# Optimization experiments

Measured on AMD Instinct MI355X. Metric: run time of the kernel, lower is better.

The kernel has to match this reference:

```python
import jax, jax.numpy as jnp
import numpy as np

H = 128          # hidden_dim
LATENT = 32
OUT = 2 * LATENT # diagonal output dist
S0, S1, S2, S3 = 65536, 16384, 4096, 1024  # HR grid, mesh0_hr/grid_lr, mesh1_hr/mesh0_lr, mesh2_hr/mesh1_lr
G = 15           # total stacked GNN blocks (HR: g2m, 2 up, 3x2 intra; LR cond: g2m, 1 up, 2x2 intra)
EDGES = {
    'hr_g2m': (131072, S0, S1), 'hr_m2m0': (131072, S1, S1),
    'hr_m2m1': (32768, S2, S2), 'hr_m2m2': (8192, S3, S3),
    'hr_up0': (65536, S1, S2), 'hr_up1': (16384, S2, S3),
    'lr_g2m': (65536, S1, S2), 'lr_m2m0': (32768, S2, S2),
    'lr_m2m1': (8192, S3, S3), 'lr_up0': (16384, S2, S3),
}


def setup_inputs():
    keys = iter(jax.random.split(jax.random.key(0), 80))
    inp = {}
    inp['high_emb'] = jax.random.normal(next(keys), (S0, H), jnp.float32)
    inp['low_emb'] = jax.random.normal(next(keys), (S1, H), jnp.float32)
    for name, n in [('hr_mesh0', S1), ('hr_mesh1', S2), ('hr_mesh2', S3), ('lr_mesh0', S2), ('lr_mesh1', S3)]:
        inp[name] = jax.random.normal(next(keys), (n, H), jnp.float32)
    for name, (e, ns, nr) in EDGES.items():
        inp[name + '_feat'] = jax.random.normal(next(keys), (e, H), jnp.float32)
        inp[name + '_src'] = jax.random.randint(next(keys), (e,), 0, ns, jnp.int32)
        inp[name + '_dst'] = jax.random.randint(next(keys), (e,), 0, nr, jnp.int32)
    s = 0.05
    inp['eW1'] = jax.random.normal(next(keys), (G, 3 * H, H), jnp.float32) * s
    inp['eb1'] = jnp.zeros((G, H), jnp.float32)
    inp['eW2'] = jax.random.normal(next(keys), (G, H, H), jnp.float32) * s
    inp['eb2'] = jnp.zeros((G, H), jnp.float32)
    inp['eln_s'] = jnp.ones((G, H), jnp.float32)
    inp['eln_b'] = jnp.zeros((G, H), jnp.float32)
    inp['nW1'] = jax.random.normal(next(keys), (G, 2 * H, H), jnp.float32) * s
    inp['nb1'] = jnp.zeros((G, H), jnp.float32)
    inp['nW2'] = jax.random.normal(next(keys), (G, H, H), jnp.float32) * s
    inp['nb2'] = jnp.zeros((G, H), jnp.float32)
    inp['nln_s'] = jnp.ones((G, H), jnp.float32)
    inp['nln_b'] = jnp.zeros((G, H), jnp.float32)
    inp['pW1'] = jax.random.normal(next(keys), (H, H), jnp.float32) * s
    inp['pb1'] = jnp.zeros((H,), jnp.float32)
    inp['pW2'] = jax.random.normal(next(keys), (H, OUT), jnp.float32) * s
    inp['pb2'] = jnp.zeros((OUT,), jnp.float32)
    return inp


def _mlp2(x, W1, b1, W2, b2, ls, lb):
    # make_mlp: Linear -> SiLU -> Linear -> LayerNorm
    h = jax.nn.silu(x @ W1 + b1) @ W2 + b2
    m = jnp.mean(h, axis=-1, keepdims=True)
    v = jnp.var(h, axis=-1, keepdims=True)
    return (h - m) * jax.lax.rsqrt(v + 1e-5) * ls + lb


def _gnn(i, send, recv, edge, src, dst, P):
    # InteractionNet/PropagationNet block i: gather -> edge MLP -> scatter-sum -> node MLP, residual updates.
    eW1, eb1, eW2, eb2, els, elb, nW1, nb1, nW2, nb2, nls, nlb = P
    e_in = jnp.concatenate([edge, send[src], recv[dst]], axis=-1)  # (E, 3H)
    e_up = _mlp2(e_in, eW1[i], eb1[i], eW2[i], eb2[i], els[i], elb[i])
    aggr = jax.ops.segment_sum(e_up, dst, num_segments=recv.shape[0])  # (Nr, H)
    n_up = _mlp2(jnp.concatenate([recv, aggr], axis=-1), nW1[i], nb1[i], nW2[i], nb2[i], nls[i], nlb[i])
    return recv + n_up, edge + e_up


def _intra(i0, rep, edge, src, dst, P):
    # make_gnn_seq: intra_level_layers=2 sequential same-level GNNs, edges updated between layers
    for i in (i0, i0 + 1):
        rep, edge = _gnn(i, rep, rep, edge, src, dst, P)
    return rep, edge


def reference(high_emb, low_emb, hr_mesh0, hr_mesh1, hr_mesh2, lr_mesh0, lr_mesh1,
              hr_g2m_feat, hr_m2m0_feat, hr_m2m1_feat, hr_m2m2_feat, hr_up0_feat, hr_up1_feat,
              lr_g2m_feat, lr_m2m0_feat, lr_m2m1_feat, lr_up0_feat,
              eW1, eb1, eW2, eb2, eln_s, eln_b, nW1, nb1, nW2, nb2, nln_s, nln_b,
              pW1, pb1, pW2, pb2,
              hr_g2m_src, hr_g2m_dst, hr_m2m0_src, hr_m2m0_dst, hr_m2m1_src, hr_m2m1_dst,
              hr_m2m2_src, hr_m2m2_dst, hr_up0_src, hr_up0_dst, hr_up1_src, hr_up1_dst,
              lr_g2m_src, lr_g2m_dst, lr_m2m0_src, lr_m2m0_dst, lr_m2m1_src, lr_m2m1_dst,
              lr_up0_src, lr_up0_dst):
    P = (eW1, eb1, eW2, eb2, eln_s, eln_b, nW1, nb1, nW2, nb2, nln_s, nln_b)
    # grid -> mesh level 0 (HR stream)
    hr_rep, _ = _gnn(0, high_emb, hr_mesh0, hr_g2m_feat, hr_g2m_src, hr_g2m_dst, P)
    hr_in, _ = _intra(3, hr_rep, hr_m2m0_feat, hr_m2m0_src, hr_m2m0_dst, P)
    rep = hr_in + low_emb
    # --- level 0 ---
    hr_up, _ = _gnn(1, rep, hr_mesh1, hr_up0_feat, hr_up0_src, hr_up0_dst, P)
    lr_up_rep0, _ = _gnn(9, low_emb, lr_mesh0, lr_g2m_feat, lr_g2m_src, lr_g2m_dst, P)  # conditioner g2m
    rep = hr_up + lr_up_rep0
    hr_in, _ = _intra(5, rep, hr_m2m1_feat, hr_m2m1_src, hr_m2m1_dst, P)
    lr_in0, _ = _intra(11, lr_up_rep0, lr_m2m0_feat, lr_m2m0_src, lr_m2m0_dst, P)  # conditioner intra[0]
    rep = hr_in + lr_in0
    # --- level 1 ---
    hr_up, _ = _gnn(2, rep, hr_mesh2, hr_up1_feat, hr_up1_src, hr_up1_dst, P)
    lr_up_rep1, _ = _gnn(10, lr_in0, lr_mesh1, lr_up0_feat, lr_up0_src, lr_up0_dst, P)  # conditioner mesh_up[0]
    rep = hr_up + lr_up_rep1
    hr_in, _ = _intra(7, rep, hr_m2m2_feat, hr_m2m2_src, hr_m2m2_dst, P)
    lr_in1, _ = _intra(13, lr_up_rep1, lr_m2m1_feat, lr_m2m1_src, lr_m2m1_dst, P)  # conditioner intra[1]
    rep = hr_in + lr_in1
    # latent_param_map: [H, H, OUT], no layer norm
    params = jax.nn.silu(rep @ pW1 + pb1) @ pW2 + pb2  # (S3, OUT)
    mu = params[:, :LATENT]
    std = 1e-4 + jax.nn.softplus(params[:, LATENT:])
    # (Normal(mu, std), skip_ins=[low_emb, lr_in0, lr_in1], skip_ups=[lr_up_rep0, lr_up_rep1])
    return (mu, std, low_emb, lr_in0, lr_in1, lr_up_rep0, lr_up_rep1)
```

## Files before the change

kernel.cpp:

```cpp
#include <hip/hip_runtime.h>
#include <hip/hip_bf16.h>

#define H 128
constexpr int S1 = 16384, S2 = 4096, S3 = 1024;

typedef unsigned short u16;
typedef float  f32x4 __attribute__((ext_vector_type(4)));
typedef short  s16x8 __attribute__((ext_vector_type(8)));
typedef __bf16 bf16x8 __attribute__((ext_vector_type(8)));

__device__ inline u16 f2bf(float f){
  unsigned u = __builtin_bit_cast(unsigned, f);
  u += 0x7FFFu + ((u >> 16) & 1u);
  return (u16)(u >> 16);
}
__device__ inline float bf2f(u16 b){ return __builtin_bit_cast(float, (unsigned)b << 16); }
__device__ inline float ldf(const u16* p, size_t i){ return bf2f(p[i]); }
__device__ inline float ldf(const float* p, size_t i){ return p[i]; }

__device__ inline s16x8 ldfrag(const u16* p, int k){
  return *reinterpret_cast<const s16x8*>(p + k);
}
__device__ inline s16x8 ldfrag(const float* p, int k){
  f32x4 f0 = *reinterpret_cast<const f32x4*>(p + k);
  f32x4 f1 = *reinterpret_cast<const f32x4*>(p + k + 4);
  s16x8 r;
  r[0]=(short)f2bf(f0[0]); r[1]=(short)f2bf(f0[1]); r[2]=(short)f2bf(f0[2]); r[3]=(short)f2bf(f0[3]);
  r[4]=(short)f2bf(f1[0]); r[5]=(short)f2bf(f1[1]); r[6]=(short)f2bf(f1[2]); r[7]=(short)f2bf(f1[3]);
  return r;
}
__device__ inline f32x4 mfma16(s16x8 a, s16x8 b, f32x4 c){
  return __builtin_amdgcn_mfma_f32_16x16x32_bf16(
      __builtin_bit_cast(bf16x8, a), __builtin_bit_cast(bf16x8, b), c, 0, 0, 0);
}

template<typename FT, bool WE>
__global__ __launch_bounds__(256) void edge_gnn(
    const FT* __restrict__ feat,
    const float* __restrict__ send, const float* __restrict__ recv,
    const int* __restrict__ src, const int* __restrict__ dst,
    const u16* __restrict__ W1T, const u16* __restrict__ W2T,
    const float* __restrict__ b1, const float* __restrict__ b2,
    const float* __restrict__ lns, const float* __restrict__ lnb,
    float* __restrict__ aggr, u16* __restrict__ eout)
{
  __shared__ u16 h1s[64*128];
  const int tid = threadIdx.x, lane = tid & 63, w = tid >> 6;
  const int l16 = lane & 15, lg = lane >> 4;
  const int eA = blockIdx.x*64 + w*16 + l16;
  const int sA = src[eA], dA = dst[eA];
  const FT* fRow = feat + (size_t)eA*H;
  const float* sRow = send + (size_t)sA*H;
  const float* rRow = recv + (size_t)dA*H;

  f32x4 acc[8];
#pragma unroll
  for(int n=0;n<8;n++) acc[n] = f32x4{0.f,0.f,0.f,0.f};

#pragma unroll
  for(int kk=0; kk<12; kk++){
    const int kq = kk*32 + lg*8;
    const int kl = (kk&3)*32 + lg*8;
    s16x8 a;
    if(kk<4)      a = ldfrag(fRow, kl);
    else if(kk<8) a = ldfrag(sRow, kl);
    else          a = ldfrag(rRow, kl);
#pragma unroll
    for(int n=0;n<8;n++){
      s16x8 b = *reinterpret_cast<const s16x8*>(W1T + (size_t)(n*16+l16)*384 + kq);
      acc[n] = mfma16(a,b,acc[n]);
    }
  }

  const int r0 = w*16 + lg*4;
#pragma unroll
  for(int n=0;n<8;n++){
    const int c = n*16 + l16;
    const float bb = b1[c];
#pragma unroll
    for(int j=0;j<4;j++){
      const int r = r0 + j;
      float x = acc[n][j] + bb;
      float sv = x / (1.f + __expf(-x));
      h1s[r*128 + (((c>>3)^(r&7))<<3) + (c&7)] = f2bf(sv);
    }
  }
  __syncthreads();

  f32x4 acc2[8];
#pragma unroll
  for(int n=0;n<8;n++) acc2[n] = f32x4{0.f,0.f,0.f,0.f};
  const int rA = w*16 + l16;
#pragma unroll
  for(int kk=0;kk<4;kk++){
    const int kq = kk*32 + lg*8;
    s16x8 a = *reinterpret_cast<const s16x8*>(&h1s[rA*128 + (((kq>>3)^(rA&7))<<3)]);
#pragma unroll
    for(int n=0;n<8;n++){
      s16x8 b = *reinterpret_cast<const s16x8*>(W2T + (size_t)(n*16+l16)*128 + kq);
      acc2[n] = mfma16(a,b,acc2[n]);
    }
  }

  float hv[8][4];
#pragma unroll
  for(int n=0;n<8;n++){
    const float bb = b2[n*16+l16];
#pragma unroll
    for(int j=0;j<4;j++) hv[n][j] = acc2[n][j] + bb;
  }
  float mj[4], rj[4];
#pragma unroll
  for(int j=0;j<4;j++){
    float s=0.f, q=0.f;
#pragma unroll
    for(int n=0;n<8;n++){ float v=hv[n][j]; s+=v; q+=v*v; }
#pragma unroll
    for(int off=1; off<16; off<<=1){ s += __shfl_xor(s, off); q += __shfl_xor(q, off); }
    const float m = s * (1.f/128.f);
    mj[j] = m;
    float var = q*(1.f/128.f) - m*m;
    rj[j] = rsqrtf((var > 0.f ? var : 0.f) + 1e-5f);
  }
#pragma unroll
  for(int n=0;n<8;n++){
    const int c = n*16+l16;
    const float sc = lns[c];
    const float bo = lnb[c];
#pragma unroll
    for(int j=0;j<4;j++) hv[n][j] = (hv[n][j]-mj[j])*rj[j]*sc + bo;
  }

#pragma unroll
  for(int j=0;j<4;j++){
    const int er = blockIdx.x*64 + r0 + j;
    const int dj = dst[er];
    float* ab = aggr + (size_t)dj*H;
#pragma unroll
    for(int n=0;n<8;n++) atomicAdd(ab + n*16 + l16, hv[n][j]);
    if(WE){
      const size_t eb = (size_t)er*H;
#pragma unroll
      for(int n=0;n<8;n++){
        const int c = n*16+l16;
        eout[eb + c] = f2bf(ldf(feat, eb + c) + hv[n][j]);
      }
    }
  }
}

__global__ __launch_bounds__(256) void node_gnn(
    const float* __restrict__ recv, const float* __restrict__ aggr,
    const u16* __restrict__ W1T, const u16* __restrict__ W2T,
    const float* __restrict__ b1, const float* __restrict__ b2,
    const float* __restrict__ lns, const float* __restrict__ lnb,
    float* __restrict__ out)
{
  __shared__ u16 h1s[64*128];
  const int tid = threadIdx.x, lane = tid & 63, w = tid >> 6;
  const int l16 = lane & 15, lg = lane >> 4;
  const int nA = blockIdx.x*64 + w*16 + l16;
  const float* rRow = recv + (size_t)nA*H;
  const float* aRow = aggr + (size_t)nA*H;

  f32x4 acc[8];
#pragma unroll
  for(int n=0;n<8;n++) acc[n] = f32x4{0.f,0.f,0.f,0.f};
#pragma unroll
  for(int kk=0; kk<8; kk++){
    const int kq = kk*32 + lg*8;
    const int kl = (kk&3)*32 + lg*8;
    s16x8 a = (kk<4) ? ldfrag(rRow, kl) : ldfrag(aRow, kl);
#pragma unroll
    for(int n=0;n<8;n++){
      s16x8 b = *reinterpret_cast<const s16x8*>(W1T + (size_t)(n*16+l16)*256 + kq);
      acc[n] = mfma16(a,b,acc[n]);
    }
  }

  const int r0 = w*16 + lg*4;
#pragma unroll
  for(int n=0;n<8;n++){
    const int c = n*16 + l16;
    const float bb = b1[c];
#pragma unroll
    for(int j=0;j<4;j++){
      const int r = r0 + j;
      float x = acc[n][j] + bb;
      float sv = x / (1.f + __expf(-x));
      h1s[r*128 + (((c>>3)^(r&7))<<3) + (c&7)] = f2bf(sv);
    }
  }
  __syncthreads();

  f32x4 acc2[8];
#pragma unroll
  for(int n=0;n<8;n++) acc2[n] = f32x4{0.f,0.f,0.f,0.f};
  const int rA = w*16 + l16;
#pragma unroll
  for(int kk=0;kk<4;kk++){
    const int kq = kk*32 + lg*8;
    s16x8 a = *reinterpret_cast<const s16x8*>(&h1s[rA*128 + (((kq>>3)^(rA&7))<<3)]);
#pragma unroll
    for(int n=0;n<8;n++){
      s16x8 b = *reinterpret_cast<const s16x8*>(W2T + (size_t)(n*16+l16)*128 + kq);
      acc2[n] = mfma16(a,b,acc2[n]);
    }
  }

  float hv[8][4];
#pragma unroll
  for(int n=0;n<8;n++){
    const float bb = b2[n*16+l16];
#pragma unroll
    for(int j=0;j<4;j++) hv[n][j] = acc2[n][j] + bb;
  }
  float mj[4], rj[4];
#pragma unroll
  for(int j=0;j<4;j++){
    float s=0.f, q=0.f;
#pragma unroll
    for(int n=0;n<8;n++){ float v=hv[n][j]; s+=v; q+=v*v; }
#pragma unroll
    for(int off=1; off<16; off<<=1){ s += __shfl_xor(s, off); q += __shfl_xor(q, off); }
    const float m = s * (1.f/128.f);
    mj[j] = m;
    float var = q*(1.f/128.f) - m*m;
    rj[j] = rsqrtf((var > 0.f ? var : 0.f) + 1e-5f);
  }
#pragma unroll
  for(int j=0;j<4;j++){
    const int nr = blockIdx.x*64 + r0 + j;
#pragma unroll
    for(int n=0;n<8;n++){
      const int c = n*16+l16;
      out[(size_t)nr*H + c] = recv[(size_t)nr*H + c] + (hv[n][j]-mj[j])*rj[j]*lns[c] + lnb[c];
    }
  }
}

__global__ __launch_bounds__(256) void decoder_k(
    const float* __restrict__ rep, const u16* __restrict__ W1T, const u16* __restrict__ W2T,
    const float* __restrict__ b1, const float* __restrict__ b2,
    float* __restrict__ outp)
{
  __shared__ u16 h1s[64*128];
  const int tid = threadIdx.x, lane = tid & 63, w = tid >> 6;
  const int l16 = lane & 15, lg = lane >> 4;
  const int nA = blockIdx.x*64 + w*16 + l16;
  const float* rRow = rep + (size_t)nA*H;

  f32x4 acc[8];
#pragma unroll
  for(int n=0;n<8;n++) acc[n] = f32x4{0.f,0.f,0.f,0.f};
#pragma unroll
  for(int kk=0;kk<4;kk++){
    const int kq = kk*32 + lg*8;
    s16x8 a = ldfrag(rRow, kq);
#pragma unroll
    for(int n=0;n<8;n++){
      s16x8 b = *reinterpret_cast<const s16x8*>(W1T + (size_t)(n*16+l16)*128 + kq);
      acc[n] = mfma16(a,b,acc[n]);
    }
  }
  const int r0 = w*16 + lg*4;
#pragma unroll
  for(int n=0;n<8;n++){
    const int c = n*16 + l16;
    const float bb = b1[c];
#pragma unroll
    for(int j=0;j<4;j++){
      const int r = r0 + j;
      float x = acc[n][j] + bb;
      float sv = x / (1.f + __expf(-x));
      h1s[r*128 + (((c>>3)^(r&7))<<3) + (c&7)] = f2bf(sv);
    }
  }
  __syncthreads();

  f32x4 acc2[4];
#pragma unroll
  for(int n=0;n<4;n++) acc2[n] = f32x4{0.f,0.f,0.f,0.f};
  const int rA = w*16 + l16;
#pragma unroll
  for(int kk=0;kk<4;kk++){
    const int kq = kk*32 + lg*8;
    s16x8 a = *reinterpret_cast<const s16x8*>(&h1s[rA*128 + (((kq>>3)^(rA&7))<<3)]);
#pragma unroll
    for(int n=0;n<4;n++){
      s16x8 b = *reinterpret_cast<const s16x8*>(W2T + (size_t)(n*16+l16)*128 + kq);
      acc2[n] = mfma16(a,b,acc2[n]);
    }
  }
#pragma unroll
  for(int n=0;n<4;n++){
    const int c = n*16 + l16;
    const float bb = b2[c];
#pragma unroll
    for(int j=0;j<4;j++){
      const int row = blockIdx.x*64 + r0 + j;
      float p = acc2[n][j] + bb;
      if(n<2){
        outp[(size_t)row*32 + c] = p;
      } else {
        float sp = (p>0.f) ? (p + log1pf(__expf(-p))) : log1pf(__expf(p));
        outp[32768 + (size_t)row*32 + (c-32)] = 1e-4f + sp;
      }
    }
  }
}

__global__ void transpose_w(const float* __restrict__ in, u16* __restrict__ out, int G, int K, int N){
  long long t = (long long)blockIdx.x*256 + threadIdx.x;
  if(t >= (long long)G*K*N) return;
  int g = (int)(t / ((long long)K*N));
  int r = (int)(t - (long long)g*K*N);
  int k = r / N, n = r - k*N;
  out[(long long)g*N*K + (long long)n*K + k] = f2bf(in[t]);
}
__global__ void add_k(const float* __restrict__ a, const float* __restrict__ b, float* __restrict__ o, int n){
  int i = blockIdx.x*256 + threadIdx.x;
  if(i<n) o[i] = a[i] + b[i];
}
__global__ void copy16(const uint4* __restrict__ in, uint4* __restrict__ out, int n16){
  int i = blockIdx.x*256 + threadIdx.x;
  if(i<n16) out[i] = in[i];
}

struct GnnCtx {
  const u16 *eW1T,*eW2T,*nW1T,*nW2T;
  const float *eb1,*eb2,*els,*elb,*nb1,*nb2,*nls,*nlb;
  float* aggr;
  hipStream_t stream;
};

template<typename FT>
static void run_gnn(const GnnCtx& C, int g, const FT* feat,
                    const float* send, const float* recv,
                    const int* src, const int* dst, int E, int Nr, u16* eout, float* nout)
{
  hipMemsetAsync(C.aggr, 0, (size_t)Nr*H*sizeof(float), C.stream);
  const u16* w1 = C.eW1T + (size_t)g*128*384;
  const u16* w2 = C.eW2T + (size_t)g*128*128;
  const u16* v1 = C.nW1T + (size_t)g*128*256;
  const u16* v2 = C.nW2T + (size_t)g*128*128;
  const float *b1=C.eb1+g*H, *b2=C.eb2+g*H, *ls=C.els+g*H, *lb=C.elb+g*H;
  const float *c1=C.nb1+g*H, *c2=C.nb2+g*H, *ms=C.nls+g*H, *mb=C.nlb+g*H;
  if(eout)
    edge_gnn<FT,true ><<<E/64,256,0,C.stream>>>(feat,send,recv,src,dst,w1,w2,b1,b2,ls,lb,C.aggr,eout);
  else
    edge_gnn<FT,false><<<E/64,256,0,C.stream>>>(feat,send,recv,src,dst,w1,w2,b1,b2,ls,lb,C.aggr,nullptr);
  node_gnn<<<Nr/64,256,0,C.stream>>>(recv,C.aggr,v1,v2,c1,c2,ms,mb,nout);
}

extern "C" void kernel_launch(void* const* d_in, const int* in_sizes, int n_in,
                              void* d_out, int out_size, void* d_ws, size_t ws_size,
                              hipStream_t stream) {
  (void)in_sizes; (void)n_in; (void)out_size; (void)ws_size;
  auto fp = [&](int i){ return (const float*)d_in[i]; };
  auto ip = [&](int i){ return (const int*)d_in[i]; };

  const float *highE=fp(0), *lowE=fp(1), *hm1=fp(3), *hm2=fp(4), *lm0=fp(5), *lm1=fp(6);
  const float *hm0=fp(2);

  char* cur = (char*)d_ws;
  auto allocF = [&](size_t n){ float* p=(float*)cur; cur += n*sizeof(float); return p; };
  auto allocU = [&](size_t n){ u16* p=(u16*)cur; size_t b = n*2; b = (b+255)&~(size_t)255; cur += b; return p; };

  u16* eW1T = allocU((size_t)15*128*384);
  u16* eW2T = allocU((size_t)15*128*128);
  u16* nW1T = allocU((size_t)15*128*256);
  u16* nW2T = allocU((size_t)15*128*128);
  u16* pW1T = allocU((size_t)128*128);
  u16* pW2T = allocU((size_t)64*128);
  float* aggr = allocF((size_t)S1*H);
  float* RA = allocF((size_t)S1*H);
  float* RB = allocF((size_t)S1*H);
  u16* Ebig = allocU((size_t)131072*H);
  u16* E1 = Ebig;
  u16* E2 = Ebig + (size_t)32768*H;
  u16* E3 = Ebig + (size_t)2*32768*H;
  u16* E4 = E3   + (size_t)8192*H;
  float* SA = allocF((size_t)S2*H);
  float* SB = allocF((size_t)S2*H);
  float* SC = allocF((size_t)S2*H);
  float* TA = allocF((size_t)S3*H);
  float* TB = allocF((size_t)S3*H);
  float* TC = allocF((size_t)S3*H);

  float* outp = (float*)d_out;
  const size_t O_LOW=65536, O_LIN0=2162688, O_LIN1=2686976, O_LUP0=2818048, O_LUP1=3342336;
  float* L0 = outp + O_LUP0;
  float* L1 = outp + O_LIN0;
  float* L2 = outp + O_LUP1;
  float* L3 = outp + O_LIN1;

  auto T = [&](int idx, u16* out, int G,int K,int N){
    long long tot = (long long)G*K*N;
    transpose_w<<<(unsigned)((tot+255)/256),256,0,stream>>>((const float*)d_in[idx], out, G,K,N);
  };
  T(37, eW1T, 15,384,128);
  T(39, eW2T, 15,128,128);
  T(43, nW1T, 15,256,128);
  T(45, nW2T, 15,128,128);
  T(49, pW1T, 1,128,128);
  T(51, pW2T, 1,128,64);

  GnnCtx C{eW1T,eW2T,nW1T,nW2T,
           fp(38),fp(40),fp(41),fp(42),fp(44),fp(46),fp(47),fp(48),
           aggr, stream};

  run_gnn(C, 0, fp(7), highE, hm0, ip(8), ip(9), 131072, S1, (u16*)nullptr, RA);
  run_gnn(C, 3, fp(10), RA, RA, ip(11), ip(12), 131072, S1, Ebig, RB);
  run_gnn(C, 4, (const u16*)Ebig, RB, RB, ip(11), ip(12), 131072, S1, (u16*)nullptr, RA);
  add_k<<<(S1*H+255)/256,256,0,stream>>>(RA, lowE, RB, S1*H);
  run_gnn(C, 1, fp(19), RB, hm1, ip(20), ip(21), 65536, S2, (u16*)nullptr, SA);
  run_gnn(C, 9, fp(25), lowE, lm0, ip(26), ip(27), 65536, S2, (u16*)nullptr, L0);
  add_k<<<(S2*H+255)/256,256,0,stream>>>(SA, L0, SB, S2*H);
  run_gnn(C, 5, fp(13), SB, SB, ip(14), ip(15), 32768, S2, E1, SC);
  run_gnn(C, 6, (const u16*)E1, SC, SC, ip(14), ip(15), 32768, S2, (u16*)nullptr, SA);
  run_gnn(C, 11, fp(28), L0, L0, ip(29), ip(30), 32768, S2, E2, SB);
  run_gnn(C, 12, (const u16*)E2, SB, SB, ip(29), ip(30), 32768, S2, (u16*)nullptr, L1);
  add_k<<<(S2*H+255)/256,256,0,stream>>>(SA, L1, SC, S2*H);
  run_gnn(C, 2, fp(22), SC, hm2, ip(23), ip(24), 16384, S3, (u16*)nullptr, TA);
  run_gnn(C, 10, fp(34), L1, lm1, ip(35), ip(36), 16384, S3, (u16*)nullptr, L2);
  add_k<<<(S3*H+255)/256,256,0,stream>>>(TA, L2, TB, S3*H);
  run_gnn(C, 7, fp(16), TB, TB, ip(17), ip(18), 8192, S3, E3, TC);
  run_gnn(C, 8, (const u16*)E3, TC, TC, ip(17), ip(18), 8192, S3, (u16*)nullptr, TA);
  run_gnn(C, 13, fp(31), L2, L2, ip(32), ip(33), 8192, S3, E4, TB);
  run_gnn(C, 14, (const u16*)E4, TB, TB, ip(32), ip(33), 8192, S3, (u16*)nullptr, L3);
  add_k<<<(S3*H+255)/256,256,0,stream>>>(TA, L3, TC, S3*H);

  decoder_k<<<S3/64,256,0,stream>>>(TC, pW1T, pW2T, fp(50), fp(52), outp);

  copy16<<<((S1*H/4)+255)/256,256,0,stream>>>((const uint4*)lowE, (uint4*)(outp+O_LOW), S1*H/4);
}
```

Baseline: 1.763 ms.

## Replace atomic scatter-add aggregation with CSR gather built once per call

Edge kernels now write their normalized updates as bf16 into a per-edge buffer instead of doing fp32 atomicAdds into node aggregates. A CSR (histogram, scan, scatter) over all ten edge sets is built at the start of each call, and a new aggr_k kernel gathers and sums each node's incoming edges. The per-block memsets are dropped, and A fragments are preloaded into registers in the MLP kernels. This trades atomic contention for extra kernels, an extra bf16 round-trip of edge updates, and rounding edge outputs to bf16 before summation.

```diff
diff --git a/kernel.cpp b/kernel.cpp
--- a/kernel.cpp
+++ b/kernel.cpp
@@ -42,7 +42,7 @@
     const u16* __restrict__ W1T, const u16* __restrict__ W2T,
     const float* __restrict__ b1, const float* __restrict__ b2,
     const float* __restrict__ lns, const float* __restrict__ lnb,
-    float* __restrict__ aggr, u16* __restrict__ eout)
+    u16* __restrict__ eup, u16* __restrict__ eout)
 {
   __shared__ u16 h1s[64*128];
   const int tid = threadIdx.x, lane = tid & 63, w = tid >> 6;
@@ -53,6 +53,14 @@
   const float* sRow = send + (size_t)sA*H;
   const float* rRow = recv + (size_t)dA*H;
 
+  s16x8 af[12];
+#pragma unroll
+  for(int kk=0;kk<4;kk++) af[kk]   = ldfrag(fRow, kk*32 + lg*8);
+#pragma unroll
+  for(int kk=0;kk<4;kk++) af[4+kk] = ldfrag(sRow, kk*32 + lg*8);
+#pragma unroll
+  for(int kk=0;kk<4;kk++) af[8+kk] = ldfrag(rRow, kk*32 + lg*8);
+
   f32x4 acc[8];
 #pragma unroll
   for(int n=0;n<8;n++) acc[n] = f32x4{0.f,0.f,0.f,0.f};
@@ -60,15 +68,10 @@
 #pragma unroll
   for(int kk=0; kk<12; kk++){
     const int kq = kk*32 + lg*8;
-    const int kl = (kk&3)*32 + lg*8;
-    s16x8 a;
-    if(kk<4)      a = ldfrag(fRow, kl);
-    else if(kk<8) a = ldfrag(sRow, kl);
-    else          a = ldfrag(rRow, kl);
 #pragma unroll
     for(int n=0;n<8;n++){
       s16x8 b = *reinterpret_cast<const s16x8*>(W1T + (size_t)(n*16+l16)*384 + kq);
-      acc[n] = mfma16(a,b,acc[n]);
+      acc[n] = mfma16(af[kk],b,acc[n]);
     }
   }
 
@@ -122,31 +125,34 @@
     float var = q*(1.f/128.f) - m*m;
     rj[j] = rsqrtf((var > 0.f ? var : 0.f) + 1e-5f);
   }
-#pragma unroll
-  for(int n=0;n<8;n++){
-    const int c = n*16+l16;
-    const float sc = lns[c];
-    const float bo = lnb[c];
-#pragma unroll
-    for(int j=0;j<4;j++) hv[n][j] = (hv[n][j]-mj[j])*rj[j]*sc + bo;
-  }
 
 #pragma unroll
   for(int j=0;j<4;j++){
     const int er = blockIdx.x*64 + r0 + j;
-    const int dj = dst[er];
-    float* ab = aggr + (size_t)dj*H;
-#pragma unroll
-    for(int n=0;n<8;n++) atomicAdd(ab + n*16 + l16, hv[n][j]);
-    if(WE){
-      const size_t eb = (size_t)er*H;
-#pragma unroll
-      for(int n=0;n<8;n++){
-        const int c = n*16+l16;
-        eout[eb + c] = f2bf(ldf(feat, eb + c) + hv[n][j]);
-      }
-    }
-  }
+    const size_t eb = (size_t)er*H;
+#pragma unroll
+    for(int n=0;n<8;n++){
+      const int c = n*16+l16;
+      const float v = (hv[n][j]-mj[j])*rj[j]*lns[c] + lnb[c];
+      eup[eb + c] = f2bf(v);
+      if(WE) eout[eb + c] = f2bf(ldf(feat, eb + c) + v);
+    }
+  }
+}
+
+__global__ __launch_bounds__(256) void aggr_k(
+    const u16* __restrict__ eup, const int* __restrict__ rowptr,
+    const int* __restrict__ elist, float* __restrict__ aggr)
+{
+  const int n = blockIdx.x*2 + (threadIdx.x>>7);
+  const int col = threadIdx.x & 127;
+  const int b = rowptr[n], e = rowptr[n+1];
+  float s = 0.f;
+  for(int i=b;i<e;i++){
+    const int eid = elist[i];
+    s += bf2f(eup[(size_t)eid*H + col]);
+  }
+  aggr[(size_t)n*H + col] = s;
 }
 
 __global__ __launch_bounds__(256) void node_gnn(
@@ -163,18 +169,22 @@
   const float* rRow = recv + (size_t)nA*H;
   const float* aRow = aggr + (size_t)nA*H;
 
+  s16x8 af[8];
+#pragma unroll
+  for(int kk=0;kk<4;kk++) af[kk]   = ldfrag(rRow, kk*32 + lg*8);
+#pragma unroll
+  for(int kk=0;kk<4;kk++) af[4+kk] = ldfrag(aRow, kk*32 + lg*8);
+
   f32x4 acc[8];
 #pragma unroll
   for(int n=0;n<8;n++) acc[n] = f32x4{0.f,0.f,0.f,0.f};
 #pragma unroll
   for(int kk=0; kk<8; kk++){
     const int kq = kk*32 + lg*8;
-    const int kl = (kk&3)*32 + lg*8;
-    s16x8 a = (kk<4) ? ldfrag(rRow, kl) : ldfrag(aRow, kl);
 #pragma unroll
     for(int n=0;n<8;n++){
       s16x8 b = *reinterpret_cast<const s16x8*>(W1T + (size_t)(n*16+l16)*256 + kq);
-      acc[n] = mfma16(a,b,acc[n]);
+      acc[n] = mfma16(af[kk],b,acc[n]);
     }
   }
 
@@ -250,17 +260,20 @@
   const int nA = blockIdx.x*64 + w*16 + l16;
   const float* rRow = rep + (size_t)nA*H;
 
+  s16x8 af[4];
+#pragma unroll
+  for(int kk=0;kk<4;kk++) af[kk] = ldfrag(rRow, kk*32 + lg*8);
+
   f32x4 acc[8];
 #pragma unroll
   for(int n=0;n<8;n++) acc[n] = f32x4{0.f,0.f,0.f,0.f};
 #pragma unroll
   for(int kk=0;kk<4;kk++){
     const int kq = kk*32 + lg*8;
-    s16x8 a = ldfrag(rRow, kq);
 #pragma unroll
     for(int n=0;n<8;n++){
       s16x8 b = *reinterpret_cast<const s16x8*>(W1T + (size_t)(n*16+l16)*128 + kq);
-      acc[n] = mfma16(a,b,acc[n]);
+      acc[n] = mfma16(af[kk],b,acc[n]);
     }
   }
   const int r0 = w*16 + lg*4;
@@ -310,6 +323,59 @@
   }
 }
 
+struct GDesc {
+  const int* dst[10];
+  int eoff[11];
+  int noff[10];
+};
+
+__global__ void hist_all(GDesc D, int* __restrict__ cnt, int Etot){
+  int t = blockIdx.x*256 + threadIdx.x;
+  if(t >= Etot) return;
+  int g = 0;
+#pragma unroll
+  for(int i=1;i<10;i++) if(t >= D.eoff[i]) g = i;
+  atomicAdd(&cnt[D.noff[g] + D.dst[g][t - D.eoff[g]]], 1);
+}
+
+__global__ void scat_all(GDesc D, int* __restrict__ cursor, int* __restrict__ elist, int Etot){
+  int t = blockIdx.x*256 + threadIdx.x;
+  if(t >= Etot) return;
+  int g = 0;
+#pragma unroll
+  for(int i=1;i<10;i++) if(t >= D.eoff[i]) g = i;
+  const int el = t - D.eoff[g];
+  const int pos = atomicAdd(&cursor[D.noff[g] + D.dst[g][el]], 1);
+  elist[pos] = el;
+}
+
+__global__ void scan1(const int* __restrict__ in, int* __restrict__ out, int* __restrict__ ptot, int n){
+  __shared__ int sm[256];
+  const int i = blockIdx.x*256 + threadIdx.x;
+  int v = (i<n)? in[i] : 0;
+  sm[threadIdx.x] = v; __syncthreads();
+  for(int off=1; off<256; off<<=1){
+    int t = (threadIdx.x>=off)? sm[threadIdx.x-off] : 0; __syncthreads();
+    sm[threadIdx.x] += t; __syncthreads();
+  }
+  if(i<n) out[i] = sm[threadIdx.x] - v;
+  if(threadIdx.x==255) ptot[blockIdx.x] = sm[255];
+}
+__global__ void scan2(int* __restrict__ ptot, int nb){
+  __shared__ int sm[256];
+  int v = (threadIdx.x<nb)? ptot[threadIdx.x] : 0;
+  sm[threadIdx.x] = v; __syncthreads();
+  for(int off=1; off<256; off<<=1){
+    int t = (threadIdx.x>=off)? sm[threadIdx.x-off] : 0; __syncthreads();
+    sm[threadIdx.x] += t; __syncthreads();
+  }
+  if(threadIdx.x<nb) ptot[threadIdx.x] = sm[threadIdx.x] - v;
+}
+__global__ void scan3(int* __restrict__ out, const int* __restrict__ ptot, int n){
+  const int i = blockIdx.x*256 + threadIdx.x;
+  if(i<n) out[i] += ptot[blockIdx.x];
+}
+
 __global__ void transpose_w(const float* __restrict__ in, u16* __restrict__ out, int G, int K, int N){
   long long t = (long long)blockIdx.x*256 + threadIdx.x;
   if(t >= (long long)G*K*N) return;
@@ -330,6 +396,9 @@
 struct GnnCtx {
   const u16 *eW1T,*eW2T,*nW1T,*nW2T;
   const float *eb1,*eb2,*els,*elb,*nb1,*nb2,*nls,*nlb;
+  u16* eup;
+  const int* scan;
+  const int* elist;
   float* aggr;
   hipStream_t stream;
 };
@@ -337,9 +406,9 @@
 template<typename FT>
 static void run_gnn(const GnnCtx& C, int g, const FT* feat,
                     const float* send, const float* recv,
-                    const int* src, const int* dst, int E, int Nr, u16* eout, float* nout)
+                    const int* src, const int* dst, int E, int Nr, int noff,
+                    u16* eout, float* nout)
 {
-  hipMemsetAsync(C.aggr, 0, (size_t)Nr*H*sizeof(float), C.stream);
   const u16* w1 = C.eW1T + (size_t)g*128*384;
   const u16* w2 = C.eW2T + (size_t)g*128*128;
   const u16* v1 = C.nW1T + (size_t)g*128*256;
@@ -347,9 +416,10 @@
   const float *b1=C.eb1+g*H, *b2=C.eb2+g*H, *ls=C.els+g*H, *lb=C.elb+g*H;
   const float *c1=C.nb1+g*H, *c2=C.nb2+g*H, *ms=C.nls+g*H, *mb=C.nlb+g*H;
   if(eout)
-    edge_gnn<FT,true ><<<E/64,256,0,C.stream>>>(feat,send,recv,src,dst,w1,w2,b1,b2,ls,lb,C.aggr,eout);
+    edge_gnn<FT,true ><<<E/64,256,0,C.stream>>>(feat,send,recv,src,dst,w1,w2,b1,b2,ls,lb,C.eup,eout);
   else
-    edge_gnn<FT,false><<<E/64,256,0,C.stream>>>(feat,send,recv,src,dst,w1,w2,b1,b2,ls,lb,C.aggr,nullptr);
+    edge_gnn<FT,false><<<E/64,256,0,C.stream>>>(feat,send,recv,src,dst,w1,w2,b1,b2,ls,lb,C.eup,nullptr);
+  aggr_k<<<Nr/2,256,0,C.stream>>>(C.eup, C.scan + noff, C.elist, C.aggr);
   node_gnn<<<Nr/64,256,0,C.stream>>>(recv,C.aggr,v1,v2,c1,c2,ms,mb,nout);
 }
 
@@ -360,12 +430,12 @@
   auto fp = [&](int i){ return (const float*)d_in[i]; };
   auto ip = [&](int i){ return (const int*)d_in[i]; };
 
-  const float *highE=fp(0), *lowE=fp(1), *hm1=fp(3), *hm2=fp(4), *lm0=fp(5), *lm1=fp(6);
-  const float *hm0=fp(2);
+  const float *highE=fp(0), *lowE=fp(1), *hm0=fp(2), *hm1=fp(3), *hm2=fp(4), *lm0=fp(5), *lm1=fp(6);
 
   char* cur = (char*)d_ws;
   auto allocF = [&](size_t n){ float* p=(float*)cur; cur += n*sizeof(float); return p; };
   auto allocU = [&](size_t n){ u16* p=(u16*)cur; size_t b = n*2; b = (b+255)&~(size_t)255; cur += b; return p; };
+  auto allocI = [&](size_t n){ int* p=(int*)cur; cur += n*sizeof(int); return p; };
 
   u16* eW1T = allocU((size_t)15*128*384);
   u16* eW2T = allocU((size_t)15*128*128);
@@ -376,6 +446,7 @@
   float* aggr = allocF((size_t)S1*H);
   float* RA = allocF((size_t)S1*H);
   float* RB = allocF((size_t)S1*H);
+  u16* eup  = allocU((size_t)131072*H);
   u16* Ebig = allocU((size_t)131072*H);
   u16* E1 = Ebig;
   u16* E2 = Ebig + (size_t)32768*H;
@@ -388,6 +459,14 @@
   float* TB = allocF((size_t)S3*H);
   float* TC = allocF((size_t)S3*H);
 
+  constexpr int NTOT = 53248;
+  constexpr int ETOT = 507904;
+  int* cnt    = allocI(NTOT+1);
+  int* scanA  = allocI(NTOT+1);
+  int* cursor = allocI(NTOT+1);
+  int* ptot   = allocI(256);
+  int* elist  = allocI(ETOT);
+
   float* outp = (float*)d_out;
   const size_t O_LOW=65536, O_LIN0=2162688, O_LIN1=2686976, O_LUP0=2818048, O_LUP1=3342336;
   float* L0 = outp + O_LUP0;
@@ -406,29 +485,48 @@
   T(49, pW1T, 1,128,128);
   T(51, pW2T, 1,128,64);
 
+  GDesc D;
+  D.dst[0]=ip(9);  D.dst[1]=ip(12); D.dst[2]=ip(15); D.dst[3]=ip(18); D.dst[4]=ip(21);
+  D.dst[5]=ip(24); D.dst[6]=ip(27); D.dst[7]=ip(30); D.dst[8]=ip(33); D.dst[9]=ip(36);
+  const int Es[10] = {131072,131072,32768,8192,65536,16384,65536,32768,8192,16384};
+  const int Ns[10] = {S1,S1,S2,S3,S2,S3,S2,S2,S3,S3};
+  int eo=0, no=0, noffv[10];
+  for(int i=0;i<10;i++){ D.eoff[i]=eo; eo+=Es[i]; D.noff[i]=no; noffv[i]=no; no+=Ns[i]; }
+  D.eoff[10]=eo;
+
+  hipMemsetAsync(cnt, 0, (NTOT+1)*sizeof(int), stream);
+  hist_all<<<(ETOT+255)/256,256,0,stream>>>(D, cnt, ETOT);
+  const int SN = NTOT+1;
+  const int NB1 = (SN+255)/256;
+  scan1<<<NB1,256,0,stream>>>(cnt, scanA, ptot, SN);
+  scan2<<<1,256,0,stream>>>(ptot, NB1);
+  scan3<<<NB1,256,0,stream>>>(scanA, ptot, SN);
+  hipMemcpyAsync(cursor, scanA, SN*sizeof(int), hipMemcpyDeviceToDevice, stream);
+  scat_all<<<(ETOT+255)/256,256,0,stream>>>(D, cursor, elist, ETOT);
+
   GnnCtx C{eW1T,eW2T,nW1T,nW2T,
            fp(38),fp(40),fp(41),fp(42),fp(44),fp(46),fp(47),fp(48),
-           aggr, stream};
-
-  run_gnn(C, 0, fp(7), highE, hm0, ip(8), ip(9), 131072, S1, (u16*)nullptr, RA);
-  run_gnn(C, 3, fp(10), RA, RA, ip(11), ip(12), 131072, S1, Ebig, RB);
-  run_gnn(C, 4, (const u16*)Ebig, RB, RB, ip(11), ip(12), 131072, S1, (u16*)nullptr, RA);
+           eup, scanA, elist, aggr, stream};
+
+  run_gnn(C, 0, fp(7), highE, hm0, ip(8), ip(9), 131072, S1, noffv[0], (u16*)nullptr, RA);
+  run_gnn(C, 3, fp(10), RA, RA, ip(11), ip(12), 131072, S1, noffv[1], Ebig, RB);
+  run_gnn(C, 4, (const u16*)Ebig, RB, RB, ip(11), ip(12), 131072, S1, noffv[1], (u16*)nullptr, RA);
   add_k<<<(S1*H+255)/256,256,0,stream>>>(RA, lowE, RB, S1*H);
-  run_gnn(C, 1, fp(19), RB, hm1, ip(20), ip(21), 65536, S2, (u16*)nullptr, SA);
-  run_gnn(C, 9, fp(25), lowE, lm0, ip(26), ip(27), 65536, S2, (u16*)nullptr, L0);
+  run_gnn(C, 1, fp(19), RB, hm1, ip(20), ip(21), 65536, S2, noffv[4], (u16*)nullptr, SA);
+  run_gnn(C, 9, fp(25), lowE, lm0, ip(26), ip(27), 65536, S2, noffv[6], (u16*)nullptr, L0);
   add_k<<<(S2*H+255)/256,256,0,stream>>>(SA, L0, SB, S2*H);
-  run_gnn(C, 5, fp(13), SB, SB, ip(14), ip(15), 32768, S2, E1, SC);
-  run_gnn(C, 6, (const u16*)E1, SC, SC, ip(14), ip(15), 32768, S2, (u16*)nullptr, SA);
-  run_gnn(C, 11, fp(28), L0, L0, ip(29), ip(30), 32768, S2, E2, SB);
-  run_gnn(C, 12, (const u16*)E2, SB, SB, ip(29), ip(30), 32768, S2, (u16*)nullptr, L1);
+  run_gnn(C, 5, fp(13), SB, SB, ip(14), ip(15), 32768, S2, noffv[2], E1, SC);
+  run_gnn(C, 6, (const u16*)E1, SC, SC, ip(14), ip(15), 32768, S2, noffv[2], (u16*)nullptr, SA);
+  run_gnn(C, 11, fp(28), L0, L0, ip(29), ip(30), 32768, S2, noffv[7], E2, SB);
+  run_gnn(C, 12, (const u16*)E2, SB, SB, ip(29), ip(30), 32768, S2, noffv[7], (u16*)nullptr, L1);
   add_k<<<(S2*H+255)/256,256,0,stream>>>(SA, L1, SC, S2*H);
-  run_gnn(C, 2, fp(22), SC, hm2, ip(23), ip(24), 16384, S3, (u16*)nullptr, TA);
-  run_gnn(C, 10, fp(34), L1, lm1, ip(35), ip(36), 16384, S3, (u16*)nullptr, L2);
+  run_gnn(C, 2, fp(22), SC, hm2, ip(23), ip(24), 16384, S3, noffv[5], (u16*)nullptr, TA);
+  run_gnn(C, 10, fp(34), L1, lm1, ip(35), ip(36), 16384, S3, noffv[9], (u16*)nullptr, L2);
   add_k<<<(S3*H+255)/256,256,0,stream>>>(TA, L2, TB, S3*H);
-  run_gnn(C, 7, fp(16), TB, TB, ip(17), ip(18), 8192, S3, E3, TC);
-  run_gnn(C, 8, (const u16*)E3, TC, TC, ip(17), ip(18), 8192, S3, (u16*)nullptr, TA);
-  run_gnn(C, 13, fp(31), L2, L2, ip(32), ip(33), 8192, S3, E4, TB);
-  run_gnn(C, 14, (const u16*)E4, TB, TB, ip(32), ip(33), 8192, S3, (u16*)nullptr, L3);
+  run_gnn(C, 7, fp(16), TB, TB, ip(17), ip(18), 8192, S3, noffv[3], E3, TC);
+  run_gnn(C, 8, (const u16*)E3, TC, TC, ip(17), ip(18), 8192, S3, noffv[3], (u16*)nullptr, TA);
+  run_gnn(C, 13, fp(31), L2, L2, ip(32), ip(33), 8192, S3, noffv[8], E4, TB);
+  run_gnn(C, 14, (const u16*)E4, TB, TB, ip(32), ip(33), 8192, S3, noffv[8], (u16*)nullptr, L3);
   add_k<<<(S3*H+255)/256,256,0,stream>>>(TA, L3, TC, S3*H);
 
   decoder_k<<<S3/64,256,0,stream>>>(TC, pW1T, pW2T, fp(50), fp(52), outp);
```

After: 1.833 ms. 4.0% more time.
